# Performance work log

Hardware: AMD Instinct MI355X
Metric: run time of the kernel (lower is better)

The kernel has to match this reference:

```python
import jax, jax.numpy as jnp
import numpy as np

K = 100
TEMPERATURE = 0.1


def setup_inputs() -> dict:
    key = jax.random.key(0)
    k1, k2 = jax.random.split(key)
    x = jax.random.normal(k1, (8, 128, 60, 60), dtype=jnp.float32)
    W = jax.random.normal(k2, (128, 2 * K), dtype=jnp.float32) * 0.02  # torch Linear(k*2, d_model).weight
    b = jnp.zeros((128,), dtype=jnp.float32)
    return {"x": x, "W": W, "b": b}


def reference(x, W, b):
    x0, x1 = jnp.split(x, 2, axis=0)
    n, c, h, w = x0.shape
    hw = h * w
    # n c h w -> n (h w) c
    f0 = jnp.transpose(x0.reshape(n, c, hw), (0, 2, 1))
    f1 = jnp.transpose(x1.reshape(n, c, hw), (0, 2, 1))
    # (f0/sqrt(c)) @ (f1/sqrt(c))^T / T  ==  f0 @ f1^T / (c*T)
    sm = jnp.einsum('nld,nsd->nls', f0, f1) / (c * TEMPERATURE)
    cm = (jax.nn.softmax(sm, axis=1) * jax.nn.softmax(sm, axis=2)).reshape(n, hw * hw)
    _, topi = jax.lax.top_k(cm, K)  # (n, K)
    qindex = topi // hw
    rindex = topi % hw
    coords0 = jnp.stack([qindex % w, qindex // w], axis=-1).astype(jnp.float32) / w  # (n, K, 2) as (x, y)
    coords1 = jnp.stack([rindex % w, rindex // w], axis=-1).astype(jnp.float32) / w
    # create_meshgrid(h, w, normalized=False): (1, h*w, 2) with (x, y), row-major
    gy, gx = jnp.meshgrid(jnp.arange(h), jnp.arange(w), indexing='ij')
    grid = jnp.stack([gx, gy], axis=-1).reshape(1, hw, 2).astype(jnp.float32) / w
    offsets0 = grid[:, :, None, :] - coords0[:, None, :, :]  # (n, hw, K, 2)
    offsets1 = grid[:, :, None, :] - coords1[:, None, :, :]
    emb0 = offsets0.reshape(n, hw, 2 * K) @ W.T + b  # (n, hw, d_model)
    emb1 = offsets1.reshape(n, hw, 2 * K) @ W.T + b
    f0 = f0 + emb0
    f1 = f1 + emb1
    f = jnp.concatenate([f0, f1], axis=0)  # (2n, hw, d)
    # n (h w) d -> n d h w
    return jnp.transpose(f, (0, 2, 1)).reshape(2 * n, c, h, w)
```

## Files before the change

### kernel.cpp

```cpp
#include <hip/hip_runtime.h>

#define HW 3600
#define PADR 3712
#define NF4 900
#define CAP 16384
#define KSEL 100
#define NT 58
typedef unsigned long long U64;

using short8   = __attribute__((ext_vector_type(8))) short;
using float4v  = __attribute__((ext_vector_type(4))) float;
using float16v = __attribute__((ext_vector_type(16))) float;

__device__ __forceinline__ unsigned monof(float f) {
    unsigned b = __float_as_uint(f);
    return (b & 0x80000000u) ? ~b : (b | 0x80000000u);
}
__device__ __forceinline__ float unmonof(unsigned m) {
    return __uint_as_float((m & 0x80000000u) ? (m ^ 0x80000000u) : ~m);
}
__device__ __forceinline__ unsigned short f2bf(float f) {
    unsigned b = __float_as_uint(f);
    return (unsigned short)((b + 0x7FFFu + ((b >> 16) & 1u)) >> 16);
}
__device__ __forceinline__ float bf2f(unsigned short h) {
    return __uint_as_float(((unsigned)h) << 16);
}
__device__ __forceinline__ void async16(const void* g, void* l) {
    __builtin_amdgcn_global_load_lds((const __attribute__((address_space(1))) void*)g,
                                     (__attribute__((address_space(3))) void*)l, 16, 0, 0);
}


__global__ __launch_bounds__(256) void conv_k(
    const float* __restrict__ x,
    unsigned short* __restrict__ hiT, unsigned short* __restrict__ loT,
    unsigned* __restrict__ zero_region)
{
    int b = blockIdx.z, l0 = blockIdx.x * 64, d0 = blockIdx.y * 64;
    __shared__ float t[64][65];
    int tid = threadIdx.x;
    if (blockIdx.y == 0 && blockIdx.z == 0) {
        int base = blockIdx.x * 512;
        for (int i = tid; i < 512; i += 256) {
            int g = base + i;
            if (g < 28808) zero_region[g] = 0u;
        }
    }
#pragma unroll
    for (int r = 0; r < 4; r++) {
        int idx = tid + 256 * r;
        int d = idx >> 4, lq = idx & 15;
        int l = l0 + lq * 4;
        const float* src = x + ((size_t)b * 128 + d0 + d) * HW;
        float4 v;
        if (l + 3 < HW) v = *(const float4*)(src + l);
        else {
            v.x = (l     < HW) ? src[l]     : 0.f;
            v.y = (l + 1 < HW) ? src[l + 1] : 0.f;
            v.z = (l + 2 < HW) ? src[l + 2] : 0.f;
            v.w = (l + 3 < HW) ? src[l + 3] : 0.f;
        }
        t[lq * 4 + 0][d] = v.x; t[lq * 4 + 1][d] = v.y;
        t[lq * 4 + 2][d] = v.z; t[lq * 4 + 3][d] = v.w;
    }
    __syncthreads();
    const int rblk = l0 >> 7;
#pragma unroll
    for (int r = 0; r < 2; r++) {
        int idx = tid + 256 * r;
        int l = idx & 63, dq = idx >> 6;
        unsigned hp[4], lp[4];
#pragma unroll
        for (int j = 0; j < 4; j++) {
            float f0 = t[l][dq * 8 + 2 * j], f1 = t[l][dq * 8 + 2 * j + 1];
            unsigned short h0 = f2bf(f0), h1 = f2bf(f1);
            unsigned short g0 = f2bf(f0 - bf2f(h0)), g1 = f2bf(f1 - bf2f(h1));
            hp[j] = (unsigned)h0 | ((unsigned)h1 << 16);
            lp[j] = (unsigned)g0 | ((unsigned)g1 << 16);
        }
        size_t o = ((size_t)(b * 29 + rblk) * 16 + (d0 >> 3) + dq) * 1024
                 + (size_t)((l0 + l) & 127) * 8;
        *(uint4*)(hiT + o) = make_uint4(hp[0], hp[1], hp[2], hp[3]);
        *(uint4*)(loT + o) = make_uint4(lp[0], lp[1], lp[2], lp[3]);
    }
}

__global__ __launch_bounds__(512) void gemm_mfma_k(
    const unsigned short* __restrict__ hiT, const unsigned short* __restrict__ loT,
    float* __restrict__ den_row, float* __restrict__ den_col,
    float* __restrict__ maxvt)
{
    const int batch = blockIdx.z, bx = blockIdx.x, by = blockIdx.y;
    __shared__ __align__(16) union SU {
        unsigned short st[2][4][4][128][8];
        struct {
            float rs[128];
            float cs[128];
            unsigned mx[256];
            float pad[7680];
            float T[8192];
        } ep;
    } u;

    const int tid = threadIdx.x;
    const int lane = tid & 63, w = tid >> 6;
    const int l31 = lane & 31, h = lane >> 5;
    const int p = w >> 1, halfr = w & 1;
    const int rg = w >> 2, cg = w & 3;

    const unsigned short* psrc = (p == 0) ? hiT : (p == 1) ? loT : (p == 2) ? hiT : loT;
    const int bsel = (p < 2) ? batch : batch + 4;
    const int rblk = (p < 2) ? by : bx;
    const size_t cbase = ((size_t)(bsel * 29 + rblk) * 16) * 1024;

    float16v acc[2];
    acc[0] = (float16v)(0.f);
    acc[1] = (float16v)(0.f);

#pragma unroll
    for (int kb = 0; kb < 4; kb++) {
        const unsigned short* g = psrc + cbase + (size_t)kb * 1024 + (halfr << 9) + lane * 8;
        async16(g, &u.st[0][p][kb][halfr << 6][0]);
    }
    __syncthreads();

#pragma unroll
    for (int t = 0; t < 4; ++t) {
        const int cur = t & 1;
        if (t < 3) {
#pragma unroll
            for (int kb = 0; kb < 4; kb++) {
                const unsigned short* g = psrc + cbase + (size_t)((t + 1) * 4 + kb) * 1024
                                        + (halfr << 9) + lane * 8;
                async16(g, &u.st[cur ^ 1][p][kb][halfr << 6][0]);
            }
        }
#pragma unroll
        for (int j = 0; j < 2; j++) {
            int kb = j * 2 + h;
            short8 ah[2], al[2], bh, bl;
            ah[0] = *(const short8*)&u.st[cur][0][kb][rg * 64 + l31][0];
            ah[1] = *(const short8*)&u.st[cur][0][kb][rg * 64 + 32 + l31][0];
            al[0] = *(const short8*)&u.st[cur][1][kb][rg * 64 + l31][0];
            al[1] = *(const short8*)&u.st[cur][1][kb][rg * 64 + 32 + l31][0];
            bh    = *(const short8*)&u.st[cur][2][kb][cg * 32 + l31][0];
            bl    = *(const short8*)&u.st[cur][3][kb][cg * 32 + l31][0];
#pragma unroll
            for (int mt = 0; mt < 2; mt++) {
                acc[mt] = __builtin_amdgcn_mfma_f32_32x32x16_bf16(ah[mt], bh, acc[mt], 0, 0, 0);
                acc[mt] = __builtin_amdgcn_mfma_f32_32x32x16_bf16(ah[mt], bl, acc[mt], 0, 0, 0);
                acc[mt] = __builtin_amdgcn_mfma_f32_32x32x16_bf16(al[mt], bh, acc[mt], 0, 0, 0);
            }
        }
        __syncthreads();
    }

    if (tid < 128) { u.ep.rs[tid] = 0.f; u.ep.cs[tid] = 0.f; }
    if (tid < 256) u.ep.mx[tid] = 0u;
    __syncthreads();

    const float scale = 0.078125f;
    float* T = u.ep.T + w * 1024;
    const bool interior = (bx < 28) && (by < 28);
    const int col0 = bx * 128 + cg * 32 + l31;
    const bool cv = interior || (col0 < HW);
    float cs = 0.f;

#pragma unroll
    for (int mt = 0; mt < 2; mt++) {
#pragma unroll
        for (int reg = 0; reg < 16; reg++) {
            float v = acc[mt][reg] * scale;
            float e = cv ? __expf(v) : 0.f;
            int rloc = (reg & 3) + 8 * (reg >> 2) + 4 * h;
            bool rv = interior || (by * 128 + rg * 64 + mt * 32 + rloc < HW);
            if (rv) cs += e;
            T[rloc * 32 + (l31 ^ rloc)] = e;
        }
        __asm__ __volatile__("s_waitcnt lgkmcnt(0)" ::: "memory");
        {
            float ps = 0.f, pm = 0.f;
#pragma unroll
            for (int i = 0; i < 16; i++) {
                float tv_ = T[l31 * 32 + ((h * 16 + i) ^ l31)];
                ps += tv_;
                pm = fmaxf(pm, tv_);
            }
            ps += __shfl_xor(ps, 32);
            pm = fmaxf(pm, __shfl_xor(pm, 32));
            if (h == 0) {
                atomicAdd(&u.ep.rs[rg * 64 + mt * 32 + l31], ps);
                atomicMax(&u.ep.mx[(cg >> 1) * 128 + rg * 64 + mt * 32 + l31],
                          monof(__logf(pm)));
            }
        }
        __asm__ __volatile__("s_waitcnt lgkmcnt(0)" ::: "memory");
    }
    cs += __shfl_xor(cs, 32);
    if (h == 0) atomicAdd(&u.ep.cs[cg * 32 + l31], cs);
    __syncthreads();

    if (tid < 128) {
        int l = by * 128 + tid;
        if (l < HW) atomicAdd(&den_row[(size_t)batch * HW + l], u.ep.rs[tid]);
        int s = bx * 128 + tid;
        if (s < HW) atomicAdd(&den_col[(size_t)batch * HW + s], u.ep.cs[tid]);
    }
    if (tid < 256) {
        int tile = tid >> 7, row = tid & 127;
        int l = by * 128 + row;
        if (l < HW)
            maxvt[((size_t)batch * NT + bx * 2 + tile) * PADR + l] =
                unmonof(u.ep.mx[tile * 128 + row]);
    }
}

__global__ __launch_bounds__(256) void stat_k(
    const float* __restrict__ den_row, const float* __restrict__ den_col,
    const float* __restrict__ maxvt, float* __restrict__ keylb)
{
    const int b = blockIdx.z, tid = threadIdx.x;
    __shared__ float lncS[HW];
    __shared__ float mlsS[NT];
    for (int i = tid; i < HW; i += 256)
        lncS[i] = __logf(den_col[(size_t)b * HW + i]);
    __syncthreads();
    if (tid < NT) {
        float mx = -3.4e38f;
        int s0 = tid * 64, s1 = s0 + 64; if (s1 > HW) s1 = HW;
        for (int s = s0; s < s1; s++) mx = fmaxf(mx, lncS[s]);
        mlsS[tid] = (s0 < HW) ? mx : 1e30f;
    }
    __syncthreads();
    int j = blockIdx.x * 240 + tid;
    if (tid < 240 && j < HW) {
        const float* mvb = maxvt + (size_t)b * NT * PADR;
        float b0 = -3.4e38f, b1_ = -3.4e38f;
#pragma unroll 4
        for (int tt = 0; tt < 58; tt += 2) {
            b0  = fmaxf(b0,  2.0f * mvb[(size_t)tt * PADR + j]       - mlsS[tt]);
            b1_ = fmaxf(b1_, 2.0f * mvb[(size_t)(tt + 1) * PADR + j] - mlsS[tt + 1]);
        }
        keylb[(size_t)b * HW + j] = fmaxf(b0, b1_) - __logf(den_row[(size_t)b * HW + j]);
    }
}

__global__ __launch_bounds__(256) void tau_k(
    const float* __restrict__ keylb, float* __restrict__ tau)
{
    const int b = blockIdx.z, tid = threadIdx.x;
    __shared__ unsigned keyS[HW];
    __shared__ unsigned hist[4096];
    __shared__ unsigned hpc[256];
    __shared__ int b1S, c1S, b2S, lcnt;
    __shared__ unsigned bestS;
    __shared__ unsigned list[1024];

    for (int i = tid; i < 4096; i += 256) hist[i] = 0u;
    if (tid == 0) { lcnt = 0; bestS = 0u; }
    __syncthreads();
    for (int i = tid; i < HW; i += 256) {
        unsigned k = monof(keylb[(size_t)b * HW + i]);
        keyS[i] = k;
        atomicAdd(&hist[k >> 20], 1u);
    }
    __syncthreads();
    { unsigned s = 0; for (int j = 0; j < 16; j++) s += hist[tid * 16 + j]; hpc[tid] = s; }
    __syncthreads();
    if (tid == 0) {
        unsigned cum = 0; int cs_ = 255;
        for (; cs_ > 0; cs_--) { if (cum + hpc[cs_] >= (unsigned)KSEL) break; cum += hpc[cs_]; }
        int bb = cs_ * 16 + 15;
        for (; bb > cs_ * 16; bb--) { if (cum + hist[bb] >= (unsigned)KSEL) break; cum += hist[bb]; }
        b1S = bb; c1S = (int)cum;
    }
    __syncthreads();
    int b1 = b1S;
    for (int i = tid; i < 4096; i += 256) hist[i] = 0u;
    __syncthreads();
    for (int i = tid; i < HW; i += 256) {
        unsigned k = keyS[i];
        if ((int)(k >> 20) == b1) atomicAdd(&hist[(k >> 8) & 4095], 1u);
    }
    __syncthreads();
    { unsigned s = 0; for (int j = 0; j < 16; j++) s += hist[tid * 16 + j]; hpc[tid] = s; }
    __syncthreads();
    if (tid == 0) {
        unsigned cum = (unsigned)c1S; int cs_ = 255;
        for (; cs_ > 0; cs_--) { if (cum + hpc[cs_] >= (unsigned)KSEL) break; cum += hpc[cs_]; }
        int bb = cs_ * 16 + 15;
        for (; bb > cs_ * 16; bb--) { if (cum + hist[bb] >= (unsigned)KSEL) break; cum += hist[bb]; }
        b2S = bb;
    }
    __syncthreads();
    int b2 = b2S;
    for (int i = tid; i < HW; i += 256) {
        unsigned k = keyS[i]; int hb = (int)(k >> 20);
        if (hb > b1 || (hb == b1 && (int)((k >> 8) & 4095) >= b2)) {
            int p = atomicAdd(&lcnt, 1);
            if (p < 1024) list[p] = k;
        }
    }
    __syncthreads();
    int L = lcnt; if (L > 1024) L = 1024;
    for (int i = tid; i < L; i += 256) {
        unsigned e = list[i]; int c = 0;
        for (int j = 0; j < L; j++) c += (list[j] >= e) ? 1 : 0;
        if (c >= KSEL) atomicMax(&bestS, e);
    }
    __syncthreads();
    if (tid == 0) tau[b] = unmonof(bestS) - 3e-4f;
}

__global__ __launch_bounds__(256) void recollect_k(
    const unsigned short* __restrict__ hiT, const unsigned short* __restrict__ loT,
    const float* __restrict__ den_row, const float* __restrict__ den_col,
    const float* __restrict__ maxvt, const float* __restrict__ tau,
    uint2* __restrict__ cand, int* __restrict__ cnt)
{
    const int t = blockIdx.x, batch = blockIdx.y;
    const int tid = threadIdx.x;
    __shared__ float lnrS[HW];
    __shared__ float lncS[64];
    __shared__ int prS[2048];
    __shared__ int pcS;
    __shared__ float mnlS;

    if (tid < 64) {
        int c = t * 64 + tid;
        float lc = (c < HW) ? __logf(den_col[(size_t)batch * HW + c]) : 1e30f;
        lncS[tid] = lc;
        float mn = lc;
#pragma unroll
        for (int off = 1; off < 64; off <<= 1) mn = fminf(mn, __shfl_xor(mn, off));
        if (tid == 0) mnlS = mn;
    }
    for (int r = tid; r < HW; r += 256)
        lnrS[r] = __logf(den_row[(size_t)batch * HW + r]);
    if (tid == 0) pcS = 0;
    __syncthreads();

    const float tv = tau[batch];
    const float tvm = tv - 3e-4f;
    const float mnl = mnlS;
    const float* mv = maxvt + ((size_t)batch * NT + t) * PADR;
    for (int r = tid; r < HW; r += 256) {
        float bnd = 2.0f * mv[r] - lnrS[r] - mnl;
        if (bnd >= tvm) {
            int p = atomicAdd(&pcS, 1);
            if (p < 2048) prS[p] = r;
        }
    }
    __syncthreads();
    int pc = pcS; if (pc > 2048) pc = 2048;
    if (pc == 0) return;

    const int lane = tid & 63, w = tid >> 6;
    const int m = lane & 15, q = lane >> 4;
    const float scale = 0.078125f;
    const size_t abase = (size_t)batch * PADR * 128;
    const size_t bbase = (size_t)(batch + 4) * PADR * 128;

    for (int g = w; g * 16 < pc; g += 4) {
        int pi = g * 16 + m;
        int rowv = (pi < pc) ? prS[pi] : HW;
        float ldrv = (pi < pc) ? lnrS[rowv] : 0.f;
        size_t arow = abase + ((size_t)(rowv >> 7) * 16) * 1024 + (size_t)(rowv & 127) * 8;

        float4v acc[4];
#pragma unroll
        for (int i = 0; i < 4; i++) acc[i] = (float4v){0.f, 0.f, 0.f, 0.f};
#pragma unroll
        for (int k0 = 0; k0 < 128; k0 += 32) {
            int kb = (k0 >> 3) + q;
            short8 ah = *(const short8*)(hiT + arow + (size_t)kb * 1024);
            short8 al = *(const short8*)(loT + arow + (size_t)kb * 1024);
#pragma unroll
            for (int nt = 0; nt < 4; nt++) {
                int c = t * 64 + nt * 16 + m;
                size_t brow = bbase + ((size_t)(c >> 7) * 16 + kb) * 1024 + (size_t)(c & 127) * 8;
                short8 bh = *(const short8*)(hiT + brow);
                short8 bl = *(const short8*)(loT + brow);
                acc[nt] = __builtin_amdgcn_mfma_f32_16x16x32_bf16(ah, bh, acc[nt], 0, 0, 0);
                acc[nt] = __builtin_amdgcn_mfma_f32_16x16x32_bf16(ah, bl, acc[nt], 0, 0, 0);
                acc[nt] = __builtin_amdgcn_mfma_f32_16x16x32_bf16(al, bh, acc[nt], 0, 0, 0);
            }
        }
#pragma unroll
        for (int nt = 0; nt < 4; nt++) {
            int c = t * 64 + nt * 16 + m;
            if (c >= HW) continue;
            float ldc = lncS[nt * 16 + m];
#pragma unroll
            for (int r = 0; r < 4; r++) {
                int ri = q * 4 + r;
                if (g * 16 + ri >= pc) continue;
                int rowo = __shfl(rowv, ri);
                float ldro = __shfl(ldrv, ri);
                float v = acc[nt][r] * scale;
                float tt2 = 2.0f * v - ldro - ldc;
                if (tt2 >= tv) {
                    int p = atomicAdd(&cnt[batch], 1);
                    if (p < CAP)
                        cand[(size_t)batch * CAP + p] =
                            make_uint2(monof(tt2), (unsigned)(rowo * HW + c));
                }
            }
        }
    }
}

__global__ __launch_bounds__(1024) void select_k(
    const uint2* __restrict__ cand, const int* __restrict__ cnt,
    const float* __restrict__ W, const float* __restrict__ bias,
    float* __restrict__ cst, float* __restrict__ sxy)
{
    const int batch = blockIdx.x;
    const int tid = threadIdx.x;
    const uint2* cb = cand + (size_t)batch * CAP;
    __shared__ U64 lk[6144];
    __shared__ int topiS[KSEL];
    __shared__ float cqx[KSEL], cqy[KSEL], crx[KSEL], cry[KSEL];

    int M = cnt[batch]; if (M > CAP) M = CAP;
    const bool useL = (M <= 6144);
    if (useL)
        for (int i = tid; i < M; i += 1024) {
            uint2 e = cb[i];
            lk[i] = ((U64)e.x << 32) | (unsigned)(~e.y);
        }
    __syncthreads();
    for (int i = tid; i < M; i += 1024) {
        U64 e;
        if (useL) e = lk[i];
        else { uint2 tt = cb[i]; e = ((U64)tt.x << 32) | (unsigned)(~tt.y); }
        int r = 0;
        for (int j = 0; j < M; j++) {
            U64 o;
            if (useL) o = lk[j];
            else { uint2 tt = cb[j]; o = ((U64)tt.x << 32) | (unsigned)(~tt.y); }
            r += (o > e) ? 1 : 0;
        }
        if (r < KSEL) topiS[r] = (int)(~(unsigned)(e & 0xffffffffu));
    }
    __syncthreads();
    if (tid < KSEL) {
        int idx = topiS[tid];
        int qq = idx / HW, rr = idx - qq * HW;
        cqx[tid] = (float)(qq % 60) / 60.0f;
        cqy[tid] = (float)(qq / 60) / 60.0f;
        crx[tid] = (float)(rr % 60) / 60.0f;
        cry[tid] = (float)(rr / 60) / 60.0f;
    }
    __syncthreads();
    if (tid < 256) {
        const int d = tid & 127, hf = tid >> 7;
        const float* wrow = W + d * 200;
        float sx = 0.f, sy = 0.f, c = 0.f;
#pragma unroll 4
        for (int k = 0; k < KSEL; k++) {
            float wx = wrow[2 * k], wy = wrow[2 * k + 1];
            sx += wx; sy += wy;
            float cx = hf ? crx[k] : cqx[k];
            float cy = hf ? cry[k] : cqy[k];
            c += cx * wx + cy * wy;
        }
        cst[(hf ? (batch + 4) : batch) * 128 + d] = bias[d] - c;
        if (batch == 0 && hf == 0) { sxy[d] = sx; sxy[128 + d] = sy; }
    }
}

__global__ __launch_bounds__(256) void final_k(
    const float* __restrict__ x, const float* __restrict__ cst,
    const float* __restrict__ sxy, float* __restrict__ out)
{
    const int bd = blockIdx.x;
    const int d = bd & 127;
    const int tid = threadIdx.x;
    const float cstv = cst[bd];
    const float sx = sxy[d], sy = sxy[128 + d];
    const float4* xin = (const float4*)(x + (size_t)bd * HW);
    float4* o4 = (float4*)(out + (size_t)bd * HW);
    for (int f = tid; f < NF4; f += 256) {
        float4 v = xin[f];
        int p0 = f * 4;
        float gy = (float)(p0 / 60) / 60.0f;
        float gxb = (float)(p0 % 60);
        float add = cstv + gy * sy;
        v.x += add + ((gxb      ) / 60.0f) * sx;
        v.y += add + ((gxb + 1.f) / 60.0f) * sx;
        v.z += add + ((gxb + 2.f) / 60.0f) * sx;
        v.w += add + ((gxb + 3.f) / 60.0f) * sx;
        o4[f] = v;
    }
}

extern "C" void kernel_launch(void* const* d_in, const int* in_sizes, int n_in,
                              void* d_out, int out_size, void* d_ws, size_t ws_size,
                              hipStream_t stream)
{
    const float* x    = (const float*)d_in[0];
    const float* W    = (const float*)d_in[1];
    const float* bias = (const float*)d_in[2];
    float* out = (float*)d_out;

    char* ws = (char*)d_ws;
    float*    den_row = (float*)(ws + 0);
    float*    den_col = (float*)(ws + 57600);
    int*      cnt     = (int*)  (ws + 115200);
    float*    tau     = (float*)(ws + 115216);
    float*    keylb   = (float*)(ws + 115264);
    float*    cst     = (float*)(ws + 115264);
    float*    sxy     = (float*)(ws + 119360);
    uint2*    cand    = (uint2*)(ws + 172864);
    float*    maxvt   = (float*)(ws + 697152);
    unsigned short* hiT = (unsigned short*)(ws + 4141888);
    unsigned short* loT = (unsigned short*)(ws + 11744064);

    conv_k     <<<dim3(58, 2, 8),  256, 0, stream>>>(x, hiT, loT, (unsigned*)ws);
    gemm_mfma_k<<<dim3(29, 29, 4), 512, 0, stream>>>(hiT, loT, den_row, den_col, maxvt);
    stat_k     <<<dim3(15, 1, 4),  256, 0, stream>>>(den_row, den_col, maxvt, keylb);
    tau_k      <<<dim3(1, 1, 4),   256, 0, stream>>>(keylb, tau);
    recollect_k<<<dim3(NT, 4),     256, 0, stream>>>(hiT, loT, den_row, den_col, maxvt, tau, cand, cnt);
    select_k   <<<dim3(4),         1024, 0, stream>>>(cand, cnt, W, bias, cst, sxy);
    final_k    <<<dim3(1024),      256, 0, stream>>>(x, cst, sxy, out);
}
```

Measured before the change: 226.2 us.

## Single-buffer GEMM staging to cut LDS and stage B tile in recollect LDS

The GEMM kernel drops its double-buffered async staging for a single buffer with a sync per K-step, which shrinks LDS use and could raise occupancy but gives up load/compute overlap. Reduction scratch moves out of the union, so it can be zeroed up front without an extra barrier. The recollect kernel now async-copies the 64-column B tile (hi and lo) into shared memory once per block instead of re-reading it from global memory for every row group. This cuts redundant global loads in recollect at the cost of more LDS there.

```diff
diff --git a/kernel.cpp b/kernel.cpp
--- a/kernel.cpp
+++ b/kernel.cpp
@@ -93,15 +93,12 @@
 {
     const int batch = blockIdx.z, bx = blockIdx.x, by = blockIdx.y;
     __shared__ __align__(16) union SU {
-        unsigned short st[2][4][4][128][8];
-        struct {
-            float rs[128];
-            float cs[128];
-            unsigned mx[256];
-            float pad[7680];
-            float T[8192];
-        } ep;
+        unsigned short st[4][4][128][8];
+        float T[8192];
     } u;
+    __shared__ float rsB[128];
+    __shared__ float csB[128];
+    __shared__ unsigned mxB[2][128];
 
     const int tid = threadIdx.x;
     const int lane = tid & 63, w = tid >> 6;
@@ -109,6 +106,9 @@
     const int p = w >> 1, halfr = w & 1;
     const int rg = w >> 2, cg = w & 3;
 
+    if (tid < 128) { rsB[tid] = 0.f; csB[tid] = 0.f; }
+    if (tid < 256) mxB[tid >> 7][tid & 127] = 0u;
+
     const unsigned short* psrc = (p == 0) ? hiT : (p == 1) ? loT : (p == 2) ? hiT : loT;
     const int bsel = (p < 2) ? batch : batch + 4;
     const int rblk = (p < 2) ? by : bx;
@@ -118,34 +118,24 @@
     acc[0] = (float16v)(0.f);
     acc[1] = (float16v)(0.f);
 
-#pragma unroll
-    for (int kb = 0; kb < 4; kb++) {
-        const unsigned short* g = psrc + cbase + (size_t)kb * 1024 + (halfr << 9) + lane * 8;
-        async16(g, &u.st[0][p][kb][halfr << 6][0]);
-    }
-    __syncthreads();
-
-#pragma unroll
-    for (int t = 0; t < 4; ++t) {
-        const int cur = t & 1;
-        if (t < 3) {
-#pragma unroll
-            for (int kb = 0; kb < 4; kb++) {
-                const unsigned short* g = psrc + cbase + (size_t)((t + 1) * 4 + kb) * 1024
-                                        + (halfr << 9) + lane * 8;
-                async16(g, &u.st[cur ^ 1][p][kb][halfr << 6][0]);
-            }
-        }
+    for (int k0 = 0; k0 < 128; k0 += 32) {
+#pragma unroll
+        for (int kb = 0; kb < 4; kb++) {
+            const unsigned short* g = psrc + cbase + (size_t)((k0 >> 3) + kb) * 1024
+                                    + (halfr << 9) + lane * 8;
+            async16(g, &u.st[p][kb][halfr << 6][0]);
+        }
+        __syncthreads();
 #pragma unroll
         for (int j = 0; j < 2; j++) {
             int kb = j * 2 + h;
             short8 ah[2], al[2], bh, bl;
-            ah[0] = *(const short8*)&u.st[cur][0][kb][rg * 64 + l31][0];
-            ah[1] = *(const short8*)&u.st[cur][0][kb][rg * 64 + 32 + l31][0];
-            al[0] = *(const short8*)&u.st[cur][1][kb][rg * 64 + l31][0];
-            al[1] = *(const short8*)&u.st[cur][1][kb][rg * 64 + 32 + l31][0];
-            bh    = *(const short8*)&u.st[cur][2][kb][cg * 32 + l31][0];
-            bl    = *(const short8*)&u.st[cur][3][kb][cg * 32 + l31][0];
+            ah[0] = *(const short8*)&u.st[0][kb][rg * 64 + l31][0];
+            ah[1] = *(const short8*)&u.st[0][kb][rg * 64 + 32 + l31][0];
+            al[0] = *(const short8*)&u.st[1][kb][rg * 64 + l31][0];
+            al[1] = *(const short8*)&u.st[1][kb][rg * 64 + 32 + l31][0];
+            bh    = *(const short8*)&u.st[2][kb][cg * 32 + l31][0];
+            bl    = *(const short8*)&u.st[3][kb][cg * 32 + l31][0];
 #pragma unroll
             for (int mt = 0; mt < 2; mt++) {
                 acc[mt] = __builtin_amdgcn_mfma_f32_32x32x16_bf16(ah[mt], bh, acc[mt], 0, 0, 0);
@@ -156,12 +146,8 @@
         __syncthreads();
     }
 
-    if (tid < 128) { u.ep.rs[tid] = 0.f; u.ep.cs[tid] = 0.f; }
-    if (tid < 256) u.ep.mx[tid] = 0u;
-    __syncthreads();
-
     const float scale = 0.078125f;
-    float* T = u.ep.T + w * 1024;
+    float* T = u.T + w * 1024;
     const bool interior = (bx < 28) && (by < 28);
     const int col0 = bx * 128 + cg * 32 + l31;
     const bool cv = interior || (col0 < HW);
@@ -190,29 +176,29 @@
             ps += __shfl_xor(ps, 32);
             pm = fmaxf(pm, __shfl_xor(pm, 32));
             if (h == 0) {
-                atomicAdd(&u.ep.rs[rg * 64 + mt * 32 + l31], ps);
-                atomicMax(&u.ep.mx[(cg >> 1) * 128 + rg * 64 + mt * 32 + l31],
+                atomicAdd(&rsB[rg * 64 + mt * 32 + l31], ps);
+                atomicMax(&mxB[cg >> 1][rg * 64 + mt * 32 + l31],
                           monof(__logf(pm)));
             }
         }
         __asm__ __volatile__("s_waitcnt lgkmcnt(0)" ::: "memory");
     }
     cs += __shfl_xor(cs, 32);
-    if (h == 0) atomicAdd(&u.ep.cs[cg * 32 + l31], cs);
+    if (h == 0) atomicAdd(&csB[cg * 32 + l31], cs);
     __syncthreads();
 
     if (tid < 128) {
         int l = by * 128 + tid;
-        if (l < HW) atomicAdd(&den_row[(size_t)batch * HW + l], u.ep.rs[tid]);
+        if (l < HW) atomicAdd(&den_row[(size_t)batch * HW + l], rsB[tid]);
         int s = bx * 128 + tid;
-        if (s < HW) atomicAdd(&den_col[(size_t)batch * HW + s], u.ep.cs[tid]);
+        if (s < HW) atomicAdd(&den_col[(size_t)batch * HW + s], csB[tid]);
     }
     if (tid < 256) {
         int tile = tid >> 7, row = tid & 127;
         int l = by * 128 + row;
         if (l < HW)
             maxvt[((size_t)batch * NT + bx * 2 + tile) * PADR + l] =
-                unmonof(u.ep.mx[tile * 128 + row]);
+                unmonof(mxB[tile][row]);
     }
 }
 
@@ -326,6 +312,21 @@
     __shared__ int prS[2048];
     __shared__ int pcS;
     __shared__ float mnlS;
+    __shared__ __align__(16) unsigned short bS[2][16][64][8];
+
+    const int lane = tid & 63, w = tid >> 6;
+    const size_t bbase = (size_t)(batch + 4) * PADR * 128;
+
+    {
+        const size_t sbase = bbase + (size_t)(t >> 1) * 16 * 1024
+                           + (size_t)(t & 1) * 512 + (size_t)lane * 8;
+#pragma unroll
+        for (int s = w; s < 32; s += 4) {
+            const int buf = s >> 4, kb = s & 15;
+            const unsigned short* g = (buf ? loT : hiT) + sbase + (size_t)kb * 1024;
+            async16(g, &bS[buf][kb][0][0]);
+        }
+    }
 
     if (tid < 64) {
         int c = t * 64 + tid;
@@ -356,11 +357,9 @@
     int pc = pcS; if (pc > 2048) pc = 2048;
     if (pc == 0) return;
 
-    const int lane = tid & 63, w = tid >> 6;
     const int m = lane & 15, q = lane >> 4;
     const float scale = 0.078125f;
     const size_t abase = (size_t)batch * PADR * 128;
-    const size_t bbase = (size_t)(batch + 4) * PADR * 128;
 
     for (int g = w; g * 16 < pc; g += 4) {
         int pi = g * 16 + m;
@@ -378,10 +377,8 @@
             short8 al = *(const short8*)(loT + arow + (size_t)kb * 1024);
 #pragma unroll
             for (int nt = 0; nt < 4; nt++) {
-                int c = t * 64 + nt * 16 + m;
-                size_t brow = bbase + ((size_t)(c >> 7) * 16 + kb) * 1024 + (size_t)(c & 127) * 8;
-                short8 bh = *(const short8*)(hiT + brow);
-                short8 bl = *(const short8*)(loT + brow);
+                short8 bh = *(const short8*)&bS[0][kb][nt * 16 + m][0];
+                short8 bl = *(const short8*)&bS[1][kb][nt * 16 + m][0];
                 acc[nt] = __builtin_amdgcn_mfma_f32_16x16x32_bf16(ah, bh, acc[nt], 0, 0, 0);
                 acc[nt] = __builtin_amdgcn_mfma_f32_16x16x32_bf16(ah, bl, acc[nt], 0, 0, 0);
                 acc[nt] = __builtin_amdgcn_mfma_f32_16x16x32_bf16(al, bh, acc[nt], 0, 0, 0);
```

Result: no change. 224.6 us (-0.7%).

## Hoist LDS fragment loads before prefetch in GEMM and split recollect rows

Applied to the files above, without the earlier changes.

In the MFMA GEMM main loop, all LDS fragments for the current stage are now read right after a waitcnt and barrier, before the next stage's async copies are issued. This lets the trailing __syncthreads be dropped, leaving one barrier per stage. In recollect_k, the grid is split four ways along rows for more parallelism. Each block's 64-column B tile is staged into shared memory once via async copies instead of being re-read from global memory per row group. The costs are higher register pressure in the GEMM and redundant B staging across the four row splits.

```diff
diff --git a/kernel.cpp b/kernel.cpp
--- a/kernel.cpp
+++ b/kernel.cpp
@@ -123,11 +123,23 @@
         const unsigned short* g = psrc + cbase + (size_t)kb * 1024 + (halfr << 9) + lane * 8;
         async16(g, &u.st[0][p][kb][halfr << 6][0]);
     }
-    __syncthreads();
 
 #pragma unroll
     for (int t = 0; t < 4; ++t) {
         const int cur = t & 1;
+        __asm__ __volatile__("s_waitcnt vmcnt(0)" ::: "memory");
+        __builtin_amdgcn_s_barrier();
+        short8 fah[2][2], fal[2][2], fbh[2], fbl[2];
+#pragma unroll
+        for (int j = 0; j < 2; j++) {
+            int kb = j * 2 + h;
+            fah[j][0] = *(const short8*)&u.st[cur][0][kb][rg * 64 + l31][0];
+            fah[j][1] = *(const short8*)&u.st[cur][0][kb][rg * 64 + 32 + l31][0];
+            fal[j][0] = *(const short8*)&u.st[cur][1][kb][rg * 64 + l31][0];
+            fal[j][1] = *(const short8*)&u.st[cur][1][kb][rg * 64 + 32 + l31][0];
+            fbh[j]    = *(const short8*)&u.st[cur][2][kb][cg * 32 + l31][0];
+            fbl[j]    = *(const short8*)&u.st[cur][3][kb][cg * 32 + l31][0];
+        }
         if (t < 3) {
 #pragma unroll
             for (int kb = 0; kb < 4; kb++) {
@@ -136,26 +148,19 @@
                 async16(g, &u.st[cur ^ 1][p][kb][halfr << 6][0]);
             }
         }
+        __builtin_amdgcn_sched_barrier(0);
 #pragma unroll
         for (int j = 0; j < 2; j++) {
-            int kb = j * 2 + h;
-            short8 ah[2], al[2], bh, bl;
-            ah[0] = *(const short8*)&u.st[cur][0][kb][rg * 64 + l31][0];
-            ah[1] = *(const short8*)&u.st[cur][0][kb][rg * 64 + 32 + l31][0];
-            al[0] = *(const short8*)&u.st[cur][1][kb][rg * 64 + l31][0];
-            al[1] = *(const short8*)&u.st[cur][1][kb][rg * 64 + 32 + l31][0];
-            bh    = *(const short8*)&u.st[cur][2][kb][cg * 32 + l31][0];
-            bl    = *(const short8*)&u.st[cur][3][kb][cg * 32 + l31][0];
 #pragma unroll
             for (int mt = 0; mt < 2; mt++) {
-                acc[mt] = __builtin_amdgcn_mfma_f32_32x32x16_bf16(ah[mt], bh, acc[mt], 0, 0, 0);
-                acc[mt] = __builtin_amdgcn_mfma_f32_32x32x16_bf16(ah[mt], bl, acc[mt], 0, 0, 0);
-                acc[mt] = __builtin_amdgcn_mfma_f32_32x32x16_bf16(al[mt], bh, acc[mt], 0, 0, 0);
+                acc[mt] = __builtin_amdgcn_mfma_f32_32x32x16_bf16(fah[j][mt], fbh[j], acc[mt], 0, 0, 0);
+                acc[mt] = __builtin_amdgcn_mfma_f32_32x32x16_bf16(fah[j][mt], fbl[j], acc[mt], 0, 0, 0);
+                acc[mt] = __builtin_amdgcn_mfma_f32_32x32x16_bf16(fal[j][mt], fbh[j], acc[mt], 0, 0, 0);
             }
         }
-        __syncthreads();
-    }
-
+    }
+
+    __builtin_amdgcn_s_barrier();
     if (tid < 128) { u.ep.rs[tid] = 0.f; u.ep.cs[tid] = 0.f; }
     if (tid < 256) u.ep.mx[tid] = 0u;
     __syncthreads();
@@ -319,13 +324,29 @@
     const float* __restrict__ maxvt, const float* __restrict__ tau,
     uint2* __restrict__ cand, int* __restrict__ cnt)
 {
-    const int t = blockIdx.x, batch = blockIdx.y;
+    const int t = blockIdx.x, batch = blockIdx.y & 3, s = blockIdx.y >> 2;
+    const int r0 = s * 900;
     const int tid = threadIdx.x;
-    __shared__ float lnrS[HW];
+    __shared__ float lnrS[900];
     __shared__ float lncS[64];
-    __shared__ int prS[2048];
+    __shared__ int prS[1024];
     __shared__ int pcS;
     __shared__ float mnlS;
+    __shared__ __align__(16) unsigned short bS[2][16][64][8];
+
+    const int lane = tid & 63, w = tid >> 6;
+    const size_t bbase = (size_t)(batch + 4) * PADR * 128;
+
+    {
+        const size_t sbase = bbase + (size_t)(t >> 1) * 16 * 1024
+                           + (size_t)(t & 1) * 512 + (size_t)lane * 8;
+#pragma unroll
+        for (int sl = w; sl < 32; sl += 4) {
+            const int buf = sl >> 4, kb = sl & 15;
+            const unsigned short* g = (buf ? loT : hiT) + sbase + (size_t)kb * 1024;
+            async16(g, &bS[buf][kb][0][0]);
+        }
+    }
 
     if (tid < 64) {
         int c = t * 64 + tid;
@@ -336,8 +357,8 @@
         for (int off = 1; off < 64; off <<= 1) mn = fminf(mn, __shfl_xor(mn, off));
         if (tid == 0) mnlS = mn;
     }
-    for (int r = tid; r < HW; r += 256)
-        lnrS[r] = __logf(den_row[(size_t)batch * HW + r]);
+    for (int r = tid; r < 900; r += 256)
+        lnrS[r] = __logf(den_row[(size_t)batch * HW + r0 + r]);
     if (tid == 0) pcS = 0;
     __syncthreads();
 
@@ -345,27 +366,26 @@
     const float tvm = tv - 3e-4f;
     const float mnl = mnlS;
     const float* mv = maxvt + ((size_t)batch * NT + t) * PADR;
-    for (int r = tid; r < HW; r += 256) {
-        float bnd = 2.0f * mv[r] - lnrS[r] - mnl;
+    for (int r = tid; r < 900; r += 256) {
+        int rr = r0 + r;
+        float bnd = 2.0f * mv[rr] - lnrS[r] - mnl;
         if (bnd >= tvm) {
             int p = atomicAdd(&pcS, 1);
-            if (p < 2048) prS[p] = r;
-        }
-    }
-    __syncthreads();
-    int pc = pcS; if (pc > 2048) pc = 2048;
+            if (p < 1024) prS[p] = rr;
+        }
+    }
+    __syncthreads();
+    int pc = pcS; if (pc > 1024) pc = 1024;
     if (pc == 0) return;
 
-    const int lane = tid & 63, w = tid >> 6;
     const int m = lane & 15, q = lane >> 4;
     const float scale = 0.078125f;
     const size_t abase = (size_t)batch * PADR * 128;
-    const size_t bbase = (size_t)(batch + 4) * PADR * 128;
 
     for (int g = w; g * 16 < pc; g += 4) {
         int pi = g * 16 + m;
         int rowv = (pi < pc) ? prS[pi] : HW;
-        float ldrv = (pi < pc) ? lnrS[rowv] : 0.f;
+        float ldrv = (pi < pc) ? lnrS[rowv - r0] : 0.f;
         size_t arow = abase + ((size_t)(rowv >> 7) * 16) * 1024 + (size_t)(rowv & 127) * 8;
 
         float4v acc[4];
@@ -378,10 +398,8 @@
             short8 al = *(const short8*)(loT + arow + (size_t)kb * 1024);
 #pragma unroll
             for (int nt = 0; nt < 4; nt++) {
-                int c = t * 64 + nt * 16 + m;
-                size_t brow = bbase + ((size_t)(c >> 7) * 16 + kb) * 1024 + (size_t)(c & 127) * 8;
-                short8 bh = *(const short8*)(hiT + brow);
-                short8 bl = *(const short8*)(loT + brow);
+                short8 bh = *(const short8*)&bS[0][kb][nt * 16 + m][0];
+                short8 bl = *(const short8*)&bS[1][kb][nt * 16 + m][0];
                 acc[nt] = __builtin_amdgcn_mfma_f32_16x16x32_bf16(ah, bh, acc[nt], 0, 0, 0);
                 acc[nt] = __builtin_amdgcn_mfma_f32_16x16x32_bf16(ah, bl, acc[nt], 0, 0, 0);
                 acc[nt] = __builtin_amdgcn_mfma_f32_16x16x32_bf16(al, bh, acc[nt], 0, 0, 0);
@@ -522,7 +540,7 @@
     gemm_mfma_k<<<dim3(29, 29, 4), 512, 0, stream>>>(hiT, loT, den_row, den_col, maxvt);
     stat_k     <<<dim3(15, 1, 4),  256, 0, stream>>>(den_row, den_col, maxvt, keylb);
     tau_k      <<<dim3(1, 1, 4),   256, 0, stream>>>(keylb, tau);
-    recollect_k<<<dim3(NT, 4),     256, 0, stream>>>(hiT, loT, den_row, den_col, maxvt, tau, cand, cnt);
+    recollect_k<<<dim3(NT, 16),    256, 0, stream>>>(hiT, loT, den_row, den_col, maxvt, tau, cand, cnt);
     select_k   <<<dim3(4),         1024, 0, stream>>>(cand, cnt, W, bias, cst, sxy);
     final_k    <<<dim3(1024),      256, 0, stream>>>(x, cst, sxy, out);
 }
```

Measured after the change: 224.7 us. No clear change (-0.7%).
